# Kernel tuning notes

Measured on AMD Instinct MI355X. Metric: run time of the kernel, lower is better.

Reference implementation:

```python
import jax, jax.numpy as jnp
import numpy as np

D_MODEL = 768
NHEAD = 12
HEAD_DIM = D_MODEL // NHEAD


def setup_inputs() -> dict:
    key = jax.random.key(0)
    ks = jax.random.split(key, 9)
    B, S = 1, 4096
    scale = 1.0 / np.sqrt(D_MODEL)
    x = jax.random.normal(ks[0], (B, S, D_MODEL), dtype=jnp.float32)
    # Linear params: weight [out,in] torch convention, bias [out]
    wq = jax.random.normal(ks[1], (D_MODEL, D_MODEL), dtype=jnp.float32) * scale
    bq = jnp.zeros((D_MODEL,), dtype=jnp.float32)
    wk = jax.random.normal(ks[2], (D_MODEL, D_MODEL), dtype=jnp.float32) * scale
    bk = jnp.zeros((D_MODEL,), dtype=jnp.float32)
    wv = jax.random.normal(ks[3], (D_MODEL, D_MODEL), dtype=jnp.float32) * scale
    bv = jnp.zeros((D_MODEL,), dtype=jnp.float32)
    wo = jax.random.normal(ks[4], (D_MODEL, D_MODEL), dtype=jnp.float32) * scale
    bo = jnp.zeros((D_MODEL,), dtype=jnp.float32)
    return {"x": x, "wq": wq, "bq": bq, "wk": wk, "bk": bk,
            "wv": wv, "bv": bv, "wo": wo, "bo": bo}


def reference(x, wq, bq, wk, bk, wv, bv, wo, bo):
    B, S, D = x.shape
    H, Hd = NHEAD, HEAD_DIM
    # projections (torch Linear: x @ W^T + b)
    q = (x @ wq.T + bq).reshape(B, S, H, Hd).transpose(0, 2, 1, 3)  # [B,H,S,Hd]
    k = (x @ wk.T + bk).reshape(B, S, H, Hd).transpose(0, 2, 1, 3)
    v = (x @ wv.T + bv).reshape(B, S, H, Hd).transpose(0, 2, 1, 3)
    scores = jnp.einsum('bhsd,bhtd->bhst', q, k) / jnp.sqrt(jnp.float32(Hd))  # [B,H,S,S]
    probs = jax.nn.softmax(scores, axis=-1)
    attn = jnp.einsum('bhst,bhtd->bhsd', probs, v)  # [B,H,S,Hd]
    attn = attn.transpose(0, 2, 1, 3).reshape(B, S, D)
    return attn @ wo.T + bo
```

## Files before the change

### kernel.cpp

```cpp
#include <hip/hip_runtime.h>
#include <hip/hip_bf16.h>

typedef __attribute__((ext_vector_type(8))) __bf16 bf16x8;
typedef __attribute__((ext_vector_type(4))) __bf16 bf16x4;
typedef __attribute__((ext_vector_type(4))) float f32x4;
typedef __attribute__((ext_vector_type(16))) float f32x16;
typedef __attribute__((ext_vector_type(2))) unsigned u32x2;

#define D_MODEL 768
#define SEQ     4096
#define NH      12
#define HD      64

#define QSCALE (0.125f * 1.44269504088896f)

__device__ __forceinline__ void gload_lds16(const void* g, void* l) {
    __builtin_amdgcn_global_load_lds(
        (const __attribute__((address_space(1))) void*)g,
        (__attribute__((address_space(3))) void*)l, 16, 0, 0);
}

__device__ __forceinline__ u32x2 plswap(unsigned a, unsigned b) {
    return __builtin_amdgcn_permlane32_swap(a, b, false, false);
}

__global__ __launch_bounds__(256) void cvt_kernel(
    const float* __restrict__ x,  const float* __restrict__ wq,
    const float* __restrict__ wk, const float* __restrict__ wv,
    const float* __restrict__ wo,
    __bf16* __restrict__ xb,  __bf16* __restrict__ wqb,
    __bf16* __restrict__ wkb, __bf16* __restrict__ wvb,
    __bf16* __restrict__ wob)
{
    const int XV = SEQ * D_MODEL / 4;
    const int WV = D_MODEL * D_MODEL / 4;
    const int total = XV + 4 * WV;
    for (int i = blockIdx.x * blockDim.x + threadIdx.x; i < total;
         i += gridDim.x * blockDim.x) {
        const float* src; __bf16* dst; int j;
        if      (i < XV)          { src = x;  dst = xb;  j = i; }
        else if (i < XV + WV)     { src = wq; dst = wqb; j = i - XV; }
        else if (i < XV + 2*WV)   { src = wk; dst = wkb; j = i - XV - WV; }
        else if (i < XV + 3*WV)   { src = wv; dst = wvb; j = i - XV - 2*WV; }
        else                      { src = wo; dst = wob; j = i - XV - 3*WV; }
        float4 v = ((const float4*)src)[j];
        bf16x4 o;
        o[0] = (__bf16)v.x; o[1] = (__bf16)v.y;
        o[2] = (__bf16)v.z; o[3] = (__bf16)v.w;
        ((bf16x4*)dst)[j] = o;
    }
}

__device__ __forceinline__ void gemm128_core(
    const __bf16* __restrict__ A, const __bf16* __restrict__ B, int KD,
    f32x4 acc[4][4], __bf16 (*As)[64], __bf16 (*Bs)[64])
{
    const int t = threadIdx.x;
    const int lane = t & 63, wid = t >> 6;
    const int wm = (wid & 1) * 64, wn = (wid >> 1) * 64;
    const int lr = lane & 15, lc = lane >> 4;
    const int rl = lane >> 3;
    const int cs = (lane & 7) ^ rl;

    const __bf16* ag = A + (size_t)(wid * 32 + rl) * KD + cs * 8;
    const __bf16* bg = B + (size_t)(wid * 32 + rl) * KD + cs * 8;

    for (int kt = 0; kt < KD / 64; ++kt) {
        __syncthreads();
        #pragma unroll
        for (int i = 0; i < 4; ++i) {
            gload_lds16(ag + (size_t)i * 8 * KD + kt * 64,
                        &As[wid * 32 + i * 8][0]);
            gload_lds16(bg + (size_t)i * 8 * KD + kt * 64,
                        &Bs[wid * 32 + i * 8][0]);
        }
        __syncthreads();

        #pragma unroll
        for (int kh = 0; kh < 2; ++kh) {
            bf16x8 af[4], bfr[4];
            #pragma unroll
            for (int mi = 0; mi < 4; ++mi)
                af[mi] = *(const bf16x8*)
                    &As[wm + mi * 16 + lr][(((kh << 2) | lc) ^ (lr & 7)) * 8];
            #pragma unroll
            for (int ni = 0; ni < 4; ++ni)
                bfr[ni] = *(const bf16x8*)
                    &Bs[wn + ni * 16 + lr][(((kh << 2) | lc) ^ (lr & 7)) * 8];
            __builtin_amdgcn_s_setprio(1);
            #pragma unroll
            for (int mi = 0; mi < 4; ++mi)
                #pragma unroll
                for (int ni = 0; ni < 4; ++ni)
                    acc[mi][ni] = __builtin_amdgcn_mfma_f32_16x16x32_bf16(
                        af[mi], bfr[ni], acc[mi][ni], 0, 0, 0);
            __builtin_amdgcn_s_setprio(0);
        }
    }
}

__global__ __launch_bounds__(256) void qkv_gemm(
    const __bf16* __restrict__ xb,
    const __bf16* __restrict__ wqb, const __bf16* __restrict__ wkb,
    const __bf16* __restrict__ wvb,
    const float* __restrict__ bq, const float* __restrict__ bk,
    const float* __restrict__ bv,
    __bf16* __restrict__ Qo, __bf16* __restrict__ Ko,
    __bf16* __restrict__ Vto)
{
    __shared__ __bf16 As[128][64];
    __shared__ __bf16 Bs[128][64];
    const int bm = blockIdx.x;
    const int seg = blockIdx.y / 6, bn = blockIdx.y % 6;
    const __bf16* B  = (seg == 0) ? wqb : (seg == 1) ? wkb : wvb;
    const float* bias = (seg == 0) ? bq : (seg == 1) ? bk : bv;

    f32x4 acc[4][4] = {};
    gemm128_core(xb + (size_t)bm * 128 * D_MODEL,
                 B  + (size_t)bn * 128 * D_MODEL, D_MODEL, acc, As, Bs);

    const int t = threadIdx.x, lane = t & 63, wid = t >> 6;
    const int wm = (wid & 1) * 64, wn = (wid >> 1) * 64;
    const int lr = lane & 15, lc = lane >> 4;
    const int m0 = bm * 128 + wm, n0 = bn * 128 + wn;

    if (seg < 2) {
        __bf16* O = (seg == 0) ? Qo : Ko;
        const float sc = (seg == 0) ? QSCALE : 1.0f;
        #pragma unroll
        for (int mi = 0; mi < 4; ++mi)
            #pragma unroll
            for (int ni = 0; ni < 4; ++ni) {
                int col = n0 + ni * 16 + lr;
                float bb = bias[col];
                #pragma unroll
                for (int r = 0; r < 4; ++r)
                    O[(size_t)(m0 + mi * 16 + lc * 4 + r) * D_MODEL + col] =
                        (__bf16)((acc[mi][ni][r] + bb) * sc);
            }
    } else {
        #pragma unroll
        for (int mi = 0; mi < 4; ++mi)
            #pragma unroll
            for (int ni = 0; ni < 4; ++ni) {
                int col = n0 + ni * 16 + lr;
                float bb = bias[col];
                bf16x4 pk;
                #pragma unroll
                for (int r = 0; r < 4; ++r)
                    pk[r] = (__bf16)(acc[mi][ni][r] + bb);
                *(bf16x4*)&Vto[(size_t)col * SEQ + m0 + mi * 16 + lc * 4] = pk;
            }
    }
}

__global__ __launch_bounds__(256) void attn_kernel(
    const __bf16* __restrict__ Q, const __bf16* __restrict__ K,
    const __bf16* __restrict__ Vt, __bf16* __restrict__ Attn)
{
    __shared__ __align__(16) char LDSc[32768];
    __bf16 (*Ks)[32][64] = (__bf16(*)[32][64])(LDSc);
    __bf16 (*Vs)[64][32] = (__bf16(*)[64][32])(LDSc + 16384);
    float* Mg = (float*)LDSc;
    float* Ml = (float*)(LDSc + 16384);

    const int bid = blockIdx.x;
    const int swz = (bid & 7) * 96 + (bid >> 3);
    const int h  = swz >> 6;
    const int q0 = (swz & 63) * 64;

    const int t = threadIdx.x, lane = t & 63, wid = t >> 6;
    const int qs = wid & 1, half = wid >> 1;
    const int ql = lane & 31, hi = lane >> 5;
    const int s7 = ql & 7;
    const int v2s = (ql >> 1) & 3;

    const int krl = lane >> 3, kcs = (lane & 7) ^ (lane >> 3);
    const int vrl = lane >> 2, vcs = (lane & 3) ^ ((lane >> 3) & 3);
    const __bf16* kg = K +
        (size_t)(half * 2048 + qs * 16 + krl) * D_MODEL + h * HD + kcs * 8;
    const __bf16* vg = Vt +
        (size_t)(h * HD + qs * 32 + vrl) * SEQ + half * 2048 + vcs * 8;

    const __bf16* qrow = Q + (size_t)(q0 + qs * 32 + ql) * D_MODEL + h * HD;
    bf16x8 qf[4];
    #pragma unroll
    for (int k4 = 0; k4 < 4; ++k4)
        qf[k4] = *(const bf16x8*)&qrow[k4 * 16 + hi * 8];

    f32x16 acc0 = {}, acc1 = {};
    f32x16 lacc = {};

    gload_lds16(kg,                    &Ks[half * 2][qs * 16][0]);
    gload_lds16(kg + 8 * D_MODEL,      &Ks[half * 2][qs * 16 + 8][0]);
    gload_lds16(vg,                    &Vs[half * 2][qs * 32][0]);
    gload_lds16(vg + (size_t)16 * SEQ, &Vs[half * 2][qs * 32 + 16][0]);

    const int NT = 2048 / 32;

#define ATILE(CUR, PT, DOPF) do {                                             \
    __syncthreads();                                                          \
    if (DOPF) {                                                               \
        const __bf16* kgt = kg + (size_t)(PT) * 32 * D_MODEL;                 \
        const __bf16* vgt = vg + (PT) * 32;                                   \
        gload_lds16(kgt,               &Ks[half*2 + ((CUR)^1)][qs*16][0]);    \
        gload_lds16(kgt + 8*D_MODEL,   &Ks[half*2 + ((CUR)^1)][qs*16+8][0]);  \
        gload_lds16(vgt,               &Vs[half*2 + ((CUR)^1)][qs*32][0]);    \
        gload_lds16(vgt + (size_t)16*SEQ,                                     \
                    &Vs[half*2 + ((CUR)^1)][qs*32+16][0]);                    \
    }                                                                         \
    f32x16 st = {};                                                           \
    __builtin_amdgcn_s_setprio(1);                                            \
    _Pragma("unroll")                                                         \
    for (int k4 = 0; k4 < 4; ++k4) {                                          \
        bf16x8 kf = *(const bf16x8*)                                          \
            &Ks[half*2 + (CUR)][ql][((k4*2 + hi) ^ s7) * 8];                  \
        st = __builtin_amdgcn_mfma_f32_32x32x16_bf16(kf, qf[k4], st, 0,0,0);  \
    }                                                                         \
    __builtin_amdgcn_s_setprio(0);                                            \
                 \
    _Pragma("unroll")                                                         \
    for (int r = 0; r < 16; ++r) st[r] = exp2f(st[r]);                        \
    lacc += st;                                                               \
                                               \
    unsigned wA[4], wB[4];                                                    \
    _Pragma("unroll")                                                         \
    for (int g = 0; g < 4; ++g) {                                             \
        union { __bf16 h2[2]; unsigned u; } pa, pb;                           \
        pa.h2[0] = (__bf16)st[4*g + 0]; pa.h2[1] = (__bf16)st[4*g + 1];       \
        pb.h2[0] = (__bf16)st[4*g + 2]; pb.h2[1] = (__bf16)st[4*g + 3];       \
        wA[g] = pa.u; wB[g] = pb.u;                                           \
    }                                                                         \
    __builtin_amdgcn_s_setprio(1);                                            \
    _Pragma("unroll")                                                         \
    for (int kb = 0; kb < 2; ++kb) {                                          \
        u32x2 sA = plswap(wA[2*kb], wA[2*kb + 1]);                            \
        u32x2 sB = plswap(wB[2*kb], wB[2*kb + 1]);                            \
        union { unsigned u[4]; bf16x8 v; } fb;                                \
        fb.u[0] = sA[0]; fb.u[1] = sB[0]; fb.u[2] = sA[1]; fb.u[3] = sB[1];   \
        bf16x8 vf0 = *(const bf16x8*)                                         \
            &Vs[half*2 + (CUR)][ql][((kb*2 + hi) ^ v2s) * 8];                 \
        bf16x8 vf1 = *(const bf16x8*)                                         \
            &Vs[half*2 + (CUR)][32 + ql][((kb*2 + hi) ^ v2s) * 8];            \
        acc0 = __builtin_amdgcn_mfma_f32_32x32x16_bf16(vf0, fb.v, acc0,0,0,0);\
        acc1 = __builtin_amdgcn_mfma_f32_32x32x16_bf16(vf1, fb.v, acc1,0,0,0);\
    }                                                                         \
    __builtin_amdgcn_s_setprio(0);                                            \
} while (0)

    for (int kk = 0; kk < NT; kk += 2) {
        ATILE(0, kk + 1, 1);
        ATILE(1, kk + 2, (kk + 2 < NT));
    }
#undef ATILE

    float l_r;
    {
        float t8[8];
        #pragma unroll
        for (int i = 0; i < 8; ++i) t8[i] = lacc[i] + lacc[i + 8];
        #pragma unroll
        for (int i = 0; i < 4; ++i) t8[i] += t8[i + 4];
        l_r = (t8[0] + t8[1]) + (t8[2] + t8[3]);
        u32x2 rp = plswap(__float_as_uint(l_r), __float_as_uint(l_r));
        l_r = __uint_as_float(rp[0]) + __uint_as_float(rp[1]);
    }

    __syncthreads();
    if (half == 1) {
        float* mybuf = Mg + qs * 2048 + lane * 32;
        #pragma unroll
        for (int j = 0; j < 4; ++j) {
            f32x4 v; v[0]=acc0[4*j]; v[1]=acc0[4*j+1]; v[2]=acc0[4*j+2]; v[3]=acc0[4*j+3];
            *(f32x4*)&mybuf[(j ^ s7) * 4] = v;
        }
        #pragma unroll
        for (int j = 0; j < 4; ++j) {
            f32x4 v; v[0]=acc1[4*j]; v[1]=acc1[4*j+1]; v[2]=acc1[4*j+2]; v[3]=acc1[4*j+3];
            *(f32x4*)&mybuf[((4 + j) ^ s7) * 4] = v;
        }
        Ml[qs * 64 + lane] = l_r;
    }
    __syncthreads();
    if (half == 0) {
        float l1 = Ml[qs * 64 + lane];
        float li = 1.0f / (l_r + l1);
        const float* obuf = Mg + qs * 2048 + lane * 32;

        __bf16* orow = Attn + (size_t)(q0 + qs * 32 + ql) * D_MODEL
                       + h * HD + hi * 4;
        #pragma unroll
        for (int g = 0; g < 4; ++g) {
            f32x4 a1 = *(const f32x4*)&obuf[(g ^ s7) * 4];
            union { __bf16 h4[4]; uint2 v2; } w;
            #pragma unroll
            for (int i = 0; i < 4; ++i)
                w.h4[i] = (__bf16)((acc0[4*g+i] + a1[i]) * li);
            *(uint2*)&orow[g * 8] = w.v2;

            f32x4 b1 = *(const f32x4*)&obuf[((4 + g) ^ s7) * 4];
            #pragma unroll
            for (int i = 0; i < 4; ++i)
                w.h4[i] = (__bf16)((acc1[4*g+i] + b1[i]) * li);
            *(uint2*)&orow[32 + g * 8] = w.v2;
        }
    }
}

__global__ __launch_bounds__(256) void out_gemm(
    const __bf16* __restrict__ Ab, const __bf16* __restrict__ wob,
    const float* __restrict__ bo, float* __restrict__ out)
{
    __shared__ __bf16 As[128][64];
    __shared__ __bf16 Bs[128][64];
    const int bm = blockIdx.x, bn = blockIdx.y;
    f32x4 acc[4][4] = {};
    gemm128_core(Ab  + (size_t)bm * 128 * D_MODEL,
                 wob + (size_t)bn * 128 * D_MODEL, D_MODEL, acc, As, Bs);

    const int t = threadIdx.x, lane = t & 63, wid = t >> 6;
    const int wm = (wid & 1) * 64, wn = (wid >> 1) * 64;
    const int lr = lane & 15, lc = lane >> 4;
    const int m0 = bm * 128 + wm, n0 = bn * 128 + wn;
    #pragma unroll
    for (int mi = 0; mi < 4; ++mi)
        #pragma unroll
        for (int ni = 0; ni < 4; ++ni) {
            int col = n0 + ni * 16 + lr;
            float bb = bo[col];
            #pragma unroll
            for (int r = 0; r < 4; ++r)
                out[(size_t)(m0 + mi * 16 + lc * 4 + r) * D_MODEL + col] =
                    acc[mi][ni][r] + bb;
        }
}

extern "C" void kernel_launch(void* const* d_in, const int* in_sizes, int n_in,
                              void* d_out, int out_size, void* d_ws, size_t ws_size,
                              hipStream_t stream) {
    const float* x  = (const float*)d_in[0];
    const float* wq = (const float*)d_in[1];
    const float* bq = (const float*)d_in[2];
    const float* wk = (const float*)d_in[3];
    const float* bk = (const float*)d_in[4];
    const float* wv = (const float*)d_in[5];
    const float* bv = (const float*)d_in[6];
    const float* wo = (const float*)d_in[7];
    const float* bo = (const float*)d_in[8];

    char* ws = (char*)d_ws;
    const size_t XB_SZ = (size_t)SEQ * D_MODEL * 2;
    const size_t W_SZ  = (size_t)D_MODEL * D_MODEL * 2;
    __bf16* xb  = (__bf16*)(ws);
    __bf16* wqb = (__bf16*)(ws + XB_SZ);
    __bf16* wkb = (__bf16*)(ws + XB_SZ + W_SZ);
    __bf16* wvb = (__bf16*)(ws + XB_SZ + 2 * W_SZ);
    __bf16* wob = (__bf16*)(ws + XB_SZ + 3 * W_SZ);
    __bf16* Qb  = (__bf16*)(ws + XB_SZ + 4 * W_SZ);
    __bf16* Kb  = (__bf16*)(ws + 2 * XB_SZ + 4 * W_SZ);
    __bf16* Vtb = (__bf16*)(ws + 3 * XB_SZ + 4 * W_SZ);
    __bf16* Ab  = (__bf16*)(ws + 4 * XB_SZ + 4 * W_SZ);

    cvt_kernel<<<1024, 256, 0, stream>>>(x, wq, wk, wv, wo,
                                         xb, wqb, wkb, wvb, wob);
    qkv_gemm<<<dim3(32, 18), 256, 0, stream>>>(xb, wqb, wkb, wvb,
                                               bq, bk, bv, Qb, Kb, Vtb);
    attn_kernel<<<768, 256, 0, stream>>>(Qb, Kb, Vtb, Ab);
    out_gemm<<<dim3(32, 6), 256, 0, stream>>>(Ab, wob, bo, (float*)d_out);
}
```

Measured before the change: 152.9 us.

## Triple-buffer K/V tiles in LDS with explicit vmcnt waits

The attention loop moves from a double-buffered to a triple-buffered K/V staging scheme in LDS. The next tile's global-to-LDS loads are now issued before waiting, and a partial `s_waitcnt vmcnt(4)` plus a bare barrier replaces the full `__syncthreads`. This lets one tile's loads stay in flight while the current tile is computed, hiding global load latency. The cost is that LDS per block grows from 32KB to 48KB, which can lower the number of resident blocks per CU.

```diff
diff --git a/kernel.cpp b/kernel.cpp
--- a/kernel.cpp
+++ b/kernel.cpp
@@ -158,11 +158,11 @@
     const __bf16* __restrict__ Q, const __bf16* __restrict__ K,
     const __bf16* __restrict__ Vt, __bf16* __restrict__ Attn)
 {
-    __shared__ __align__(16) char LDSc[32768];
+    __shared__ __align__(16) char LDSc[49152];
     __bf16 (*Ks)[32][64] = (__bf16(*)[32][64])(LDSc);
-    __bf16 (*Vs)[64][32] = (__bf16(*)[64][32])(LDSc + 16384);
+    __bf16 (*Vs)[64][32] = (__bf16(*)[64][32])(LDSc + 24576);
     float* Mg = (float*)LDSc;
-    float* Ml = (float*)(LDSc + 16384);
+    float* Ml = (float*)(LDSc + 24576);
 
     const int bid = blockIdx.x;
     const int swz = (bid & 7) * 96 + (bid >> 3);
@@ -191,30 +191,33 @@
     f32x16 acc0 = {}, acc1 = {};
     f32x16 lacc = {};
 
-    gload_lds16(kg,                    &Ks[half * 2][qs * 16][0]);
-    gload_lds16(kg + 8 * D_MODEL,      &Ks[half * 2][qs * 16 + 8][0]);
-    gload_lds16(vg,                    &Vs[half * 2][qs * 32][0]);
-    gload_lds16(vg + (size_t)16 * SEQ, &Vs[half * 2][qs * 32 + 16][0]);
+    #define STAGE(BUF, TT) do {                                               \
+        const __bf16* kgt = kg + (size_t)(TT) * 32 * D_MODEL;                 \
+        const __bf16* vgt = vg + (TT) * 32;                                   \
+        gload_lds16(kgt,                    &Ks[half*3 + (BUF)][qs*16][0]);   \
+        gload_lds16(kgt + 8 * D_MODEL,      &Ks[half*3 + (BUF)][qs*16+8][0]); \
+        gload_lds16(vgt,                    &Vs[half*3 + (BUF)][qs*32][0]);   \
+        gload_lds16(vgt + (size_t)16 * SEQ, &Vs[half*3 + (BUF)][qs*32+16][0]);\
+    } while (0)
+
+    STAGE(0, 0);
 
     const int NT = 2048 / 32;
 
-#define ATILE(CUR, PT, DOPF) do {                                             \
-    __syncthreads();                                                          \
+#define ATILE(CUR, NXT, PT, DOPF) do {                                        \
     if (DOPF) {                                                               \
-        const __bf16* kgt = kg + (size_t)(PT) * 32 * D_MODEL;                 \
-        const __bf16* vgt = vg + (PT) * 32;                                   \
-        gload_lds16(kgt,               &Ks[half*2 + ((CUR)^1)][qs*16][0]);    \
-        gload_lds16(kgt + 8*D_MODEL,   &Ks[half*2 + ((CUR)^1)][qs*16+8][0]);  \
-        gload_lds16(vgt,               &Vs[half*2 + ((CUR)^1)][qs*32][0]);    \
-        gload_lds16(vgt + (size_t)16*SEQ,                                     \
-                    &Vs[half*2 + ((CUR)^1)][qs*32+16][0]);                    \
+        STAGE(NXT, PT);                                                       \
+        asm volatile("s_waitcnt vmcnt(4)" ::: "memory");                      \
+    } else {                                                                  \
+        asm volatile("s_waitcnt vmcnt(0)" ::: "memory");                      \
     }                                                                         \
+    __builtin_amdgcn_s_barrier();                                             \
     f32x16 st = {};                                                           \
     __builtin_amdgcn_s_setprio(1);                                            \
     _Pragma("unroll")                                                         \
     for (int k4 = 0; k4 < 4; ++k4) {                                          \
         bf16x8 kf = *(const bf16x8*)                                          \
-            &Ks[half*2 + (CUR)][ql][((k4*2 + hi) ^ s7) * 8];                  \
+            &Ks[half*3 + (CUR)][ql][((k4*2 + hi) ^ s7) * 8];                  \
         st = __builtin_amdgcn_mfma_f32_32x32x16_bf16(kf, qf[k4], st, 0,0,0);  \
     }                                                                         \
     __builtin_amdgcn_s_setprio(0);                                            \
@@ -239,20 +242,23 @@
         union { unsigned u[4]; bf16x8 v; } fb;                                \
         fb.u[0] = sA[0]; fb.u[1] = sB[0]; fb.u[2] = sA[1]; fb.u[3] = sB[1];   \
         bf16x8 vf0 = *(const bf16x8*)                                         \
-            &Vs[half*2 + (CUR)][ql][((kb*2 + hi) ^ v2s) * 8];                 \
+            &Vs[half*3 + (CUR)][ql][((kb*2 + hi) ^ v2s) * 8];                 \
         bf16x8 vf1 = *(const bf16x8*)                                         \
-            &Vs[half*2 + (CUR)][32 + ql][((kb*2 + hi) ^ v2s) * 8];            \
+            &Vs[half*3 + (CUR)][32 + ql][((kb*2 + hi) ^ v2s) * 8];            \
         acc0 = __builtin_amdgcn_mfma_f32_32x32x16_bf16(vf0, fb.v, acc0,0,0,0);\
         acc1 = __builtin_amdgcn_mfma_f32_32x32x16_bf16(vf1, fb.v, acc1,0,0,0);\
     }                                                                         \
     __builtin_amdgcn_s_setprio(0);                                            \
 } while (0)
 
-    for (int kk = 0; kk < NT; kk += 2) {
-        ATILE(0, kk + 1, 1);
-        ATILE(1, kk + 2, (kk + 2 < NT));
-    }
+    for (int kk = 0; kk < 63; kk += 3) {
+        ATILE(0, 1, kk + 1, 1);
+        ATILE(1, 2, kk + 2, 1);
+        ATILE(2, 0, kk + 3, (kk + 3 < NT));
+    }
+    ATILE(0, 1, 0, 0);
 #undef ATILE
+#undef STAGE
 
     float l_r;
     {
```

New measurement: 151.0 us. No clear change (-1.2%).
